# Optimization experiments

Measured on AMD Instinct MI355X. Metric: run time of the kernel, lower is better.

The kernel has to match this reference:

```python
import jax, jax.numpy as jnp
import numpy as np

NP_, NB_, E_, BE_ = 10000, 30000, 300000, 8192
PIN, BIN, EA = 128, 128, 16
HID, GH = 64, 4
D, TH, L, NC, SEQ = 128, 4, 2, 10, 6


def _ln(x, g, b, eps=1e-5):
    m = x.mean(-1, keepdims=True)
    v = ((x - m) ** 2).mean(-1, keepdims=True)
    return (x - m) * jax.lax.rsqrt(v + eps) * g + b


def _seg_softmax(e, seg, n):
    m = jax.ops.segment_max(e, seg, num_segments=n)
    m = jnp.where(jnp.isfinite(m), m, 0.0)
    ex = jnp.exp(e - m[seg])
    s = jax.ops.segment_sum(ex, seg, num_segments=n)
    return ex / (s[seg] + 1e-16)


def _gatv2(xs, xd, es, ed, ea, Wl, bl, Wr, br, We, att, bias, n_dst):
    # PyG GATv2Conv, concat=False, add_self_loops=False, eval mode (no dropout)
    xl = (xs @ Wl + bl).reshape(-1, GH, HID)   # [Ns,H,C] source transform (message content)
    xr = (xd @ Wr + br).reshape(-1, GH, HID)   # [Nd,H,C] dest transform
    eh = (ea @ We).reshape(-1, GH, HID)        # [E,H,C] edge transform (no bias in PyG)
    msg = xl[es] + xr[ed] + eh                 # [E,H,C]
    score = jnp.einsum('ehc,hc->eh', jax.nn.leaky_relu(msg, 0.2), att)
    alpha = _seg_softmax(score, ed, n_dst)     # softmax over in-edges per dest node
    out = jax.ops.segment_sum(alpha[..., None] * xl[es], ed, num_segments=n_dst)
    return out.mean(axis=1) + bias             # concat=False -> mean over heads


def _mha(x, Wqkv, bqkv, Wo, bo):
    S, d = x.shape
    dh = d // TH
    q, k, v = jnp.split(x @ Wqkv + bqkv, 3, axis=-1)
    q = q.reshape(S, TH, dh).transpose(1, 0, 2)
    k = k.reshape(S, TH, dh).transpose(1, 0, 2)
    v = v.reshape(S, TH, dh).transpose(1, 0, 2)
    a = jax.nn.softmax(jnp.einsum('hqd,hkd->hqk', q, k) / jnp.sqrt(jnp.float32(dh)), axis=-1)
    o = jnp.einsum('hqk,hkd->hqd', a, v).transpose(1, 0, 2).reshape(S, d)
    return o @ Wo + bo


def _forward(pitcher_feat, batter_feat, edge_attr, history_states,
             Wp, bp, Wb, bb,
             rel_Wl, rel_bl, rel_Wr, rel_br, rel_We, rel_att, rel_bias,
             rev_Wl, rev_bl, rev_Wr, rev_br, rev_We, rev_att, rev_bias,
             Wgs, bgs, Wet, bet, pos,
             Wqkv, bqkv, Wo, bo, ln1g, ln1b, W1, b1, W2, b2, ln2g, ln2b,
             Wc1, bc1, Wc2, bc2,
             edge_src, edge_dst, edge_ids):
    gelu = lambda t: jax.nn.gelu(t, approximate=False)
    px = gelu(pitcher_feat @ Wp + bp)
    bx = gelu(batter_feat @ Wb + bb)
    # ('pitcher','faces','batter'): messages pitcher->batter, aggregated at batter nodes
    h_b = gelu(_gatv2(px, bx, edge_src, edge_dst, edge_attr,
                      rel_Wl, rel_bl, rel_Wr, rel_br, rel_We, rel_att, rel_bias, bx.shape[0]))
    # reversed relation: batter->pitcher, aggregated at pitcher nodes
    h_p = gelu(_gatv2(bx, px, edge_dst, edge_src, edge_attr,
                      rev_Wl, rev_bl, rev_Wr, rev_br, rev_We, rev_att, rev_bias, px.shape[0]))
    state = jnp.concatenate([h_p.mean(0), h_b.mean(0), edge_attr.mean(0)], -1) @ Wgs + bgs
    tok = jnp.concatenate([h_p[edge_src[edge_ids]], h_b[edge_dst[edge_ids]],
                           edge_attr[edge_ids]], -1) @ Wet + bet
    x = jnp.concatenate([history_states, state[None]], 0) + pos[:SEQ]
    for i in range(L):  # post-LN TransformerEncoderLayer, gelu activation, eval (no dropout)
        x = _ln(x + _mha(x, Wqkv[i], bqkv[i], Wo[i], bo[i]), ln1g[i], ln1b[i])
        f = gelu(x @ W1[i] + b1[i]) @ W2[i] + b2[i]
        x = _ln(x + f, ln2g[i], ln2b[i])
    ctx = x[-1]
    cat = jnp.concatenate([tok, jnp.broadcast_to(ctx, (tok.shape[0], D))], -1)
    return gelu(cat @ Wc1 + bc1) @ Wc2 + bc2


def setup_inputs() -> dict:
    key = jax.random.key(0)
    ks = iter(jax.random.split(key, 64))
    nrm = lambda shape, s: jax.random.normal(next(ks), shape, dtype=jnp.float32) * s
    d = {
        'pitcher_feat': nrm((NP_, PIN), 1.0),
        'batter_feat': nrm((NB_, BIN), 1.0),
        'edge_attr': nrm((E_, EA), 1.0),
        'history_states': nrm((SEQ - 1, D), 1.0),
        'Wp': nrm((PIN, HID), 0.05), 'bp': jnp.zeros((HID,), jnp.float32),
        'Wb': nrm((BIN, HID), 0.05), 'bb': jnp.zeros((HID,), jnp.float32),
    }
    for p in ('rel', 'rev'):
        d[p + '_Wl'] = nrm((HID, GH * HID), 0.05)
        d[p + '_bl'] = jnp.zeros((GH * HID,), jnp.float32)
        d[p + '_Wr'] = nrm((HID, GH * HID), 0.05)
        d[p + '_br'] = jnp.zeros((GH * HID,), jnp.float32)
        d[p + '_We'] = nrm((EA, GH * HID), 0.05)
        d[p + '_att'] = nrm((GH, HID), 0.05)
        d[p + '_bias'] = jnp.zeros((HID,), jnp.float32)
    cin = 2 * HID + EA
    d['Wgs'] = nrm((cin, D), 0.05); d['bgs'] = jnp.zeros((D,), jnp.float32)
    d['Wet'] = nrm((cin, D), 0.05); d['bet'] = jnp.zeros((D,), jnp.float32)
    d['pos'] = nrm((SEQ, D), 0.02)
    d['Wqkv'] = nrm((L, D, 3 * D), 0.05); d['bqkv'] = jnp.zeros((L, 3 * D), jnp.float32)
    d['Wo'] = nrm((L, D, D), 0.05); d['bo'] = jnp.zeros((L, D), jnp.float32)
    d['ln1g'] = jnp.ones((L, D), jnp.float32); d['ln1b'] = jnp.zeros((L, D), jnp.float32)
    d['W1'] = nrm((L, D, 4 * D), 0.05); d['b1'] = jnp.zeros((L, 4 * D), jnp.float32)
    d['W2'] = nrm((L, 4 * D, D), 0.05); d['b2'] = jnp.zeros((L, D), jnp.float32)
    d['ln2g'] = jnp.ones((L, D), jnp.float32); d['ln2b'] = jnp.zeros((L, D), jnp.float32)
    d['Wc1'] = nrm((2 * D, D), 0.05); d['bc1'] = jnp.zeros((D,), jnp.float32)
    d['Wc2'] = nrm((D, NC), 0.05); d['bc2'] = jnp.zeros((NC,), jnp.float32)
    d['edge_src'] = jax.random.randint(next(ks), (E_,), 0, NP_)
    d['edge_dst'] = jax.random.randint(next(ks), (E_,), 0, NB_)
    d['edge_ids'] = jax.random.randint(next(ks), (BE_,), 0, E_)
    return d


def reference(pitcher_feat, batter_feat, edge_attr, history_states,
              Wp, bp, Wb, bb,
              rel_Wl, rel_bl, rel_Wr, rel_br, rel_We, rel_att, rel_bias,
              rev_Wl, rev_bl, rev_Wr, rev_br, rev_We, rev_att, rev_bias,
              Wgs, bgs, Wet, bet, pos,
              Wqkv, bqkv, Wo, bo, ln1g, ln1b, W1, b1, W2, b2, ln2g, ln2b,
              Wc1, bc1, Wc2, bc2,
              edge_src, edge_dst, edge_ids):
    return _forward(pitcher_feat, batter_feat, edge_attr, history_states,
                    Wp, bp, Wb, bb,
                    rel_Wl, rel_bl, rel_Wr, rel_br, rel_We, rel_att, rel_bias,
                    rev_Wl, rev_bl, rev_Wr, rev_br, rev_We, rev_att, rev_bias,
                    Wgs, bgs, Wet, bet, pos,
                    Wqkv, bqkv, Wo, bo, ln1g, ln1b, W1, b1, W2, b2, ln2g, ln2b,
                    Wc1, bc1, Wc2, bc2,
                    edge_src, edge_dst, edge_ids)
```

## Files before the change

### kernel.cpp

```cpp
#include <hip/hip_runtime.h>
#include <math.h>

#define NP 10000
#define NB 30000
#define NEDGE 300000
#define BEDGE 8192
#define EAD 16
#define HID 64
#define GH 4
#define CW 256
#define DD 128
#define SEQ 6
#define NCLS 10
#define L 2
#define NEACOL 64

#if defined(__has_builtin)
#  if __has_builtin(__builtin_amdgcn_fdot2)
#    define HAVE_DOT2 1
#  else
#    define HAVE_DOT2 0
#  endif
#else
#  define HAVE_DOT2 0
// ... 214 lines not shown
  return __builtin_bit_cast(int, __builtin_amdgcn_cvt_pkrtz(fv.x, fv.y));
}
#define GAT_PAIR(X0, X1, EV0, EV1, V1OK, P0MASK)                             \
  {                                                                          \
    float x0 = b2f(X0.x), x1 = b2f(X0.y), x2 = b2f(X0.z), x3 = b2f(X0.w);    \
    float y0 = b2f(X1.x), y1 = b2f(X1.y), y2 = b2f(X1.z), y3 = b2f(X1.w);    \
    float h00 = x0 + r0, h01 = x1 + r1, h02 = x2 + r2, h03 = x3 + r3;        \
    float h10 = y0 + r0, h11 = y1 + r1, h12 = y2 + r2, h13 = y3 + r3;        \
    _Pragma("unroll")                                                        \
    for (int j = 0; j < 8; ++j){                                             \
      int c0 = __builtin_amdgcn_readlane(EV0, j);                            \
      int c1 = __builtin_amdgcn_readlane(EV1, j);                            \
      h16x2 e0 = __builtin_bit_cast(h16x2, c0);                              \
      h16x2 e1 = __builtin_bit_cast(h16x2, c1);                              \
      int4 wr = *(const int4*)&sWeH[j*CW + 4*l];                             \
      h16x2 w0 = __builtin_bit_cast(h16x2, wr.x);                            \
      h16x2 w1 = __builtin_bit_cast(h16x2, wr.y);                            \
      h16x2 w2 = __builtin_bit_cast(h16x2, wr.z);                            \
      h16x2 w3 = __builtin_bit_cast(h16x2, wr.w);                            \
      h00 = __builtin_amdgcn_fdot2(e0, w0, h00, false);                      \
      h01 = __builtin_amdgcn_fdot2(e0, w1, h01, false);                      \
      h02 = __builtin_amdgcn_fdot2(e0, w2, h02, false);                      \
      h03 = __builtin_amdgcn_fdot2(e0, w3, h03, false);                      \
      h10 = __builtin_amdgcn_fdot2(e1, w0, h10, false);                      \
      h11 = __builtin_amdgcn_fdot2(e1, w1, h11, false);                      \
      h12 = __builtin_amdgcn_fdot2(e1, w2, h12, false);                      \
      h13 = __builtin_amdgcn_fdot2(e1, w3, h13, false);                      \
    }                                                                        \
    h00 = fmaxf(h00, 0.2f*h00) * at.x;                                       \
    h01 = fmaxf(h01, 0.2f*h01) * at.y;                                       \
    h02 = fmaxf(h02, 0.2f*h02) * at.z;                                       \
    h03 = fmaxf(h03, 0.2f*h03) * at.w;                                       \
    h10 = fmaxf(h10, 0.2f*h10) * at.x;                                       \
    h11 = fmaxf(h11, 0.2f*h11) * at.y;                                       \
    h12 = fmaxf(h12, 0.2f*h12) * at.z;                                       \
    h13 = fmaxf(h13, 0.2f*h13) * at.w;                                       \
    float g0 = (h00 + h01) + (h02 + h03);                                    \
    float g1 = (h10 + h11) + (h12 + h13);                                    \
    _Pragma("unroll")                                                        \
    for (int off = 1; off < 16; off <<= 1){                                  \
      g0 += __shfl_xor(g0, off);                                             \
      g1 += __shfl_xor(g1, off);                                             \
    }                                                                        \
    float p0 = (P0MASK) ? __expf(g0) : 0.f;                                  \
    float p1 = (V1OK) ? __expf(g1) : 0.f;                                    \
    s += p0 + p1;                                                            \
    a0 = fmaf(p0, x0, fmaf(p1, y0, a0));                                     \
    a1 = fmaf(p0, x1, fmaf(p1, y1, a1));                                     \
    a2 = fmaf(p0, x2, fmaf(p1, y2, a2));                                     \
    a3 = fmaf(p0, x3, fmaf(p1, y3, a3));                                     \
  }
#else
typedef float evt_t;
__device__ __forceinline__ float evload(const float* __restrict__ ea, int e, int l){
  return ea[(size_t)e*EAD + (l & 15)];
}
#define GAT_PAIR(X0, X1, EV0, EV1, V1OK, P0MASK)                             \
  {                                                                          \
    float x0 = b2f(X0.x), x1 = b2f(X0.y), x2 = b2f(X0.z), x3 = b2f(X0.w);    \
    float y0 = b2f(X1.x), y1 = b2f(X1.y), y2 = b2f(X1.z), y3 = b2f(X1.w);    \
    float h00 = x0 + r0, h01 = x1 + r1, h02 = x2 + r2, h03 = x3 + r3;        \
    float h10 = y0 + r0, h11 = y1 + r1, h12 = y2 + r2, h13 = y3 + r3;        \
    int ia0 = __float_as_int(EV0);                                           \
    int ia1 = __float_as_int(EV1);                                           \
    _Pragma("unroll")                                                        \
    for (int k = 0; k < EAD; ++k){                                           \
      float c0 = __int_as_float(__builtin_amdgcn_readlane(ia0, k));          \
      float c1 = __int_as_float(__builtin_amdgcn_readlane(ia1, k));          \
      float4 wv = *(const float4*)&sWeH[k*CW + 4*l];                         \
      h00 = fmaf(c0, wv.x, h00); h01 = fmaf(c0, wv.y, h01);                  \
      h02 = fmaf(c0, wv.z, h02); h03 = fmaf(c0, wv.w, h03);                  \
      h10 = fmaf(c1, wv.x, h10); h11 = fmaf(c1, wv.y, h11);                  \
      h12 = fmaf(c1, wv.z, h12); h13 = fmaf(c1, wv.w, h13);                  \
    }                                                                        \
    h00 = fmaxf(h00, 0.2f*h00) * at.x;                                       \
    h01 = fmaxf(h01, 0.2f*h01) * at.y;                                       \
    h02 = fmaxf(h02, 0.2f*h02) * at.z;                                       \
    h03 = fmaxf(h03, 0.2f*h03) * at.w;                                       \
    h10 = fmaxf(h10, 0.2f*h10) * at.x;                                       \
    h11 = fmaxf(h11, 0.2f*h11) * at.y;                                       \
    h12 = fmaxf(h12, 0.2f*h12) * at.z;                                       \
    h13 = fmaxf(h13, 0.2f*h13) * at.w;                                       \
    float g0 = (h00 + h01) + (h02 + h03);                                    \
    float g1 = (h10 + h11) + (h12 + h13);                                    \
    _Pragma("unroll")                                                        \
    for (int off = 1; off < 16; off <<= 1){                                  \
      g0 += __shfl_xor(g0, off);                                             \
      g1 += __shfl_xor(g1, off);                                             \
    }                                                                        \
    float p0 = (P0MASK) ? __expf(g0) : 0.f;                                  \
    float p1 = (V1OK) ? __expf(g1) : 0.f;                                    \
    s += p0 + p1;                                                            \
    a0 = fmaf(p0, x0, fmaf(p1, y0, a0));                                     \
    a1 = fmaf(p0, x1, fmaf(p1, y1, a1));                                     \
    a2 = fmaf(p0, x2, fmaf(p1, y2, a2));                                     \
    a3 = fmaf(p0, x3, fmaf(p1, y3, a3));                                     \
  }
#endif

__global__ __launch_bounds__(256)
void gat2_kernel(const unsigned short* __restrict__ xlA_, const unsigned short* __restrict__ xrA_,
                 const float* __restrict__ WeA, const float* __restrict__ attA,
                 const float* __restrict__ biasA, const int2* __restrict__ csrA_,
                 const int* __restrict__ rsA_, float* __restrict__ houtA,
                 const unsigned short* __restrict__ xlB_, const unsigned short* __restrict__ xrB_,
                 const float* __restrict__ WeB, const float* __restrict__ attB,
                 const float* __restrict__ biasB, const int2* __restrict__ csrB_,
                 const int* __restrict__ rsB_, float* __restrict__ houtB,
                 const float* __restrict__ ea, float* __restrict__ mvec, int gsplit)
{
#if HAVE_DOT2
  __shared__ int sWeH[8*CW];
#else
  __shared__ float sWeH[16*CW];
#endif
  __shared__ float csum[4][16][4];
  int t = threadIdx.x, l = t & 63;
  int b = blockIdx.x;
  if (b < NEACOL){
    colsum_seg(b, NEACOL, (const float4*)ea, (long)NEDGE*EAD/4, 4,
               mvec + 128, 1.f/NEDGE, &csum[0][0][0]);
    return;
  }
  b -= NEACOL;
  int ngat = (int)gridDim.x - NEACOL;
  bool isA = b < gsplit;
  const unsigned short* xl = isA ? xlA_ : xlB_;
  const unsigned short* xr = isA ? xrA_ : xrB_;
  const float* We   = isA ? WeA   : WeB;
  const float* att  = isA ? attA  : attB;
  const float* bias = isA ? biasA : biasB;
  const int2* csr   = isA ? csrA_ : csrB_;
  const int* row_start = isA ? rsA_ : rsB_;
  float* hout = isA ? houtA : houtB;
  int ndst = isA ? NB : NP;
  int bid  = isA ? b : b - gsplit;
  int nblk = isA ? gsplit : ngat - gsplit;

#if HAVE_DOT2
  for (int i = t; i < 8*CW; i += 256){
    int j = i >> 8, c = i & 255;
    sWeH[i] = __builtin_bit_cast(int,
        __builtin_amdgcn_cvt_pkrtz(We[(2*j)*CW + c], We[(2*j+1)*CW + c]));
  }
#else
  for (int i = t*4; i < 16*CW; i += 1024)
    *(float4*)&sWeH[i] = *(const float4*)&We[i];
#endif
  __syncthreads();
  float4 at = *(const float4*)&att[4*l];
  float4 bi = *(const float4*)&bias[(l & 15)*4];
  float cs0 = 0.f, cs1 = 0.f, cs2 = 0.f, cs3 = 0.f;
  int wid = bid*4 + (t >> 6);
  int nw = nblk*4;
  for (int d = wid; d < ndst; d += nw){
    ushort4 ru = *(const ushort4*)(xr + (size_t)d*CW + 4*l);
    float r0 = b2f(ru.x), r1 = b2f(ru.y), r2 = b2f(ru.z), r3 = b2f(ru.w);
    int rs = row_start[d], re = row_start[d+1];
    float s = 0.f;
    float a0 = 0.f, a1 = 0.f, a2 = 0.f, a3 = 0.f;
    if (rs < re){
      int last = re - 1;
      #define CLMP(x) ((x) > last ? last : (x))
      int2 qA0 = csr[rs],         qA1 = csr[CLMP(rs+1)];
      int2 qB0 = csr[CLMP(rs+2)], qB1 = csr[CLMP(rs+3)];
      int2 nA0 = csr[CLMP(rs+4)], nA1 = csr[CLMP(rs+5)];
      int2 nB0 = csr[CLMP(rs+6)], nB1 = csr[CLMP(rs+7)];
      ushort4 xA0 = *(const ushort4*)(xl + (size_t)qA0.y*CW + 4*l);
      ushort4 xA1 = *(const ushort4*)(xl + (size_t)qA1.y*CW + 4*l);
      evt_t  evA0 = evload(ea, qA0.x, l);
      evt_t  evA1 = evload(ea, qA1.x, l);
      ushort4 xB0 = *(const ushort4*)(xl + (size_t)qB0.y*CW + 4*l);
      ushort4 xB1 = *(const ushort4*)(xl + (size_t)qB1.y*CW + 4*l);
      evt_t  evB0 = evload(ea, qB0.x, l);
      evt_t  evB1 = evload(ea, qB1.x, l);
      for (int i = rs; i < re; i += 4){
        int2 mA0 = csr[CLMP(i+8)],  mA1 = csr[CLMP(i+9)];
        int2 mB0 = csr[CLMP(i+10)], mB1 = csr[CLMP(i+11)];
        GAT_PAIR(xA0, xA1, evA0, evA1, (i+1 < re), true);
        xA0 = *(const ushort4*)(xl + (size_t)nA0.y*CW + 4*l);
        xA1 = *(const ushort4*)(xl + (size_t)nA1.y*CW + 4*l);
        evA0 = evload(ea, nA0.x, l);
        evA1 = evload(ea, nA1.x, l);
        nA0 = mA0; nA1 = mA1;
        GAT_PAIR(xB0, xB1, evB0, evB1, (i+3 < re), (i+2 < re));
        xB0 = *(const ushort4*)(xl + (size_t)nB0.y*CW + 4*l);
        xB1 = *(const ushort4*)(xl + (size_t)nB1.y*CW + 4*l);
        evB0 = evload(ea, nB0.x, l);
        evB1 = evload(ea, nB1.x, l);
        nB0 = mB0; nB1 = mB1;
      }
      #undef CLMP
    }
    float inv = 1.f / (s + 1e-16f);
    float v0 = a0*inv, v1 = a1*inv, v2 = a2*inv, v3 = a3*inv;
    v0 += __shfl_xor(v0, 16); v1 += __shfl_xor(v1, 16);
    v2 += __shfl_xor(v2, 16); v3 += __shfl_xor(v3, 16);
    v0 += __shfl_xor(v0, 32); v1 += __shfl_xor(v1, 32);
    v2 += __shfl_xor(v2, 32); v3 += __shfl_xor(v3, 32);
    if (l < 16){
      float4 o;
      o.x = geluf(v0*0.25f + bi.x);
      o.y = geluf(v1*0.25f + bi.y);
      o.z = geluf(v2*0.25f + bi.z);
      o.w = geluf(v3*0.25f + bi.w);
      *(float4*)(hout + (size_t)d*HID + 4*l) = o;
      cs0 += o.x; cs1 += o.y; cs2 += o.z; cs3 += o.w;
    }
  }
  int w = t >> 6;
  if (l < 16){
    csum[w][l][0] = cs0; csum[w][l][1] = cs1;
    csum[w][l][2] = cs2; csum[w][l][3] = cs3;
  }
  __syncthreads();
  if (t < 64){
    int lq = t >> 2, j = t & 3;
    float sum = csum[0][lq][j] + csum[1][lq][j] + csum[2][lq][j] + csum[3][lq][j];
    float scale = isA ? (1.f/NB) : (1.f/NP);
    float* dst = isA ? (mvec + 64) : mvec;
    atomicAdd(&dst[t], sum * scale);
  }
}

__device__ void gemmcat_body(int bid, const float* __restrict__ hp, const float* __restrict__ hb,
                             const float* __restrict__ ea, const int* __restrict__ esrc,
                             const int* __restrict__ edst, const int* __restrict__ eids,
                             const float* __restrict__ W, const float* __restrict__ bias,
                             float* __restrict__ out)
{
  __shared__ float sAT[16][68];
  __shared__ float sB[16][68];
  __shared__ int sS[64], sD[64], sE[64];
  int t = threadIdx.x;
  int m0 = (bid >> 1)*64, n0 = (bid & 1)*64;
  if (t < 64){
    int e = eids[m0 + t];
    sS[t] = esrc[e]; sD[t] = edst[e]; sE[t] = e;
  }
  __syncthreads();
  int tr = t >> 4, tc = t & 15;
  float acc[4][4] = {};
  for (int k0 = 0; k0 < 144; k0 += 16){
    {
      int r = t >> 2, c = (t & 3) * 4;
      const float* src; int col = k0 + c;
      if (k0 < 64)       { src = hp + (size_t)sS[r]*HID; }
      else if (k0 < 128) { src = hb + (size_t)sD[r]*HID; col -= 64; }
      else               { src = ea + (size_t)sE[r]*EAD; col -= 128; }
      float4 va = *(const float4*)(src + col);
      sAT[c+0][r] = va.x; sAT[c+1][r] = va.y; sAT[c+2][r] = va.z; sAT[c+3][r] = va.w;
    }
    {
      int r = t >> 4, c = (t & 15) * 4;
      float4 vb = *(const float4*)(W + (size_t)(k0+r)*DD + n0 + c);
      *(float4*)&sB[r][c] = vb;
    }
    __syncthreads();
    #pragma unroll
    for (int k = 0; k < 16; ++k){
      float4 av = *(const float4*)&sAT[k][tr*4];
      float4 bv = *(const float4*)&sB[k][tc*4];
      acc[0][0] = fmaf(av.x, bv.x, acc[0][0]);
      acc[0][1] = fmaf(av.x, bv.y, acc[0][1]);
      acc[0][2] = fmaf(av.x, bv.z, acc[0][2]);
      acc[0][3] = fmaf(av.x, bv.w, acc[0][3]);
      acc[1][0] = fmaf(av.y, bv.x, acc[1][0]);
      acc[1][1] = fmaf(av.y, bv.y, acc[1][1]);
      acc[1][2] = fmaf(av.y, bv.z, acc[1][2]);
      acc[1][3] = fmaf(av.y, bv.w, acc[1][3]);
      acc[2][0] = fmaf(av.z, bv.x, acc[2][0]);
      acc[2][1] = fmaf(av.z, bv.y, acc[2][1]);
      acc[2][2] = fmaf(av.z, bv.z, acc[2][2]);
      acc[2][3] = fmaf(av.z, bv.w, acc[2][3]);
      acc[3][0] = fmaf(av.w, bv.x, acc[3][0]);
      acc[3][1] = fmaf(av.w, bv.y, acc[3][1]);
      acc[3][2] = fmaf(av.w, bv.z, acc[3][2]);
      acc[3][3] = fmaf(av.w, bv.w, acc[3][3]);
    }
    __syncthreads();
  }
  #pragma unroll
  for (int i = 0; i < 4; ++i){
    int gr = m0 + tr*4 + i;
    float4 v;
    v.x = acc[i][0] + bias[n0 + tc*4 + 0];
    v.y = acc[i][1] + bias[n0 + tc*4 + 1];
    v.z = acc[i][2] + bias[n0 + tc*4 + 2];
    v.w = acc[i][3] + bias[n0 + tc*4 + 3];
    *(float4*)(out + (size_t)gr*DD + n0 + tc*4) = v;
  }
}

__global__ __launch_bounds__(256)
void gemmcat_kernel(const float* __restrict__ hp, const float* __restrict__ hb,
                    const float* __restrict__ ea, const int* __restrict__ esrc,
                    const int* __restrict__ edst, const int* __restrict__ eids,
                    const float* __restrict__ Wet, const float* __restrict__ bet,
                    float* __restrict__ tokb)
{
  gemmcat_body(blockIdx.x, hp, hb, ea, esrc, edst, eids, Wet, bet, tokb);
}

template<int K, int N, int NC>
__device__ __forceinline__ void qstageF(const float* __restrict__ x,
                                        const float* __restrict__ W,
                                        float (&a)[6][4], int q, int ch)
{
  constexpr int NQ = N/4;
  constexpr int KC = K/NC;
  constexpr int J  = KC/4;
  const float4* wp = (const float4*)W + (size_t)(ch*KC)*NQ + q;
  const float* xb = x + ch*KC;
  float4 wv[KC];
  int kx[J];
  #pragma unroll
  for (int j = 0; j < J; ++j){
    int k4 = (j + ch) & (J-1);
    kx[j] = k4;
    wv[j*4+0] = wp[(size_t)(k4*4+0)*NQ];
    wv[j*4+1] = wp[(size_t)(k4*4+1)*NQ];
    wv[j*4+2] = wp[(size_t)(k4*4+2)*NQ];
    wv[j*4+3] = wp[(size_t)(k4*4+3)*NQ];
  }
  #pragma unroll
  for (int s = 0; s < 6; ++s){ a[s][0]=0.f; a[s][1]=0.f; a[s][2]=0.f; a[s][3]=0.f; }
  #pragma unroll
  for (int j = 0; j < J; ++j){
    #pragma unroll
    for (int s = 0; s < 6; ++s){
      float4 xv = *(const float4*)&xb[s*K + kx[j]*4];
      a[s][0]=fmaf(xv.x,wv[j*4+0].x,a[s][0]); a[s][0]=fmaf(xv.y,wv[j*4+1].x,a[s][0]);
      a[s][0]=fmaf(xv.z,wv[j*4+2].x,a[s][0]); a[s][0]=fmaf(xv.w,wv[j*4+3].x,a[s][0]);
      a[s][1]=fmaf(xv.x,wv[j*4+0].y,a[s][1]); a[s][1]=fmaf(xv.y,wv[j*4+1].y,a[s][1]);
      a[s][1]=fmaf(xv.z,wv[j*4+2].y,a[s][1]); a[s][1]=fmaf(xv.w,wv[j*4+3].y,a[s][1]);
      a[s][2]=fmaf(xv.x,wv[j*4+0].z,a[s][2]); a[s][2]=fmaf(xv.y,wv[j*4+1].z,a[s][2]);
      a[s][2]=fmaf(xv.z,wv[j*4+2].z,a[s][2]); a[s][2]=fmaf(xv.w,wv[j*4+3].z,a[s][2]);
      a[s][3]=fmaf(xv.x,wv[j*4+0].w,a[s][3]); a[s][3]=fmaf(xv.y,wv[j*4+1].w,a[s][3]);
      a[s][3]=fmaf(xv.z,wv[j*4+2].w,a[s][3]); a[s][3]=fmaf(xv.w,wv[j*4+3].w,a[s][3]);
    }
  }
  #pragma unroll
  for (int off = 1; off < NC; off <<= 1){
    #pragma unroll
    for (int s = 0; s < 6; ++s){
      a[s][0]+=__shfl_xor(a[s][0],off); a[s][1]+=__shfl_xor(a[s][1],off);
      a[s][2]+=__shfl_xor(a[s][2],off); a[s][3]+=__shfl_xor(a[s][3],off);
    }
  }
}

__global__ __launch_bounds__(512)
void xform_kernel(const float* __restrict__ hist, const float* __restrict__ mvec,
                  const float* __restrict__ Wgs, const float* __restrict__ bgs,
                  const float* __restrict__ pos,
                  const float* __restrict__ Wqkv, const float* __restrict__ bqkv,
                  const float* __restrict__ Wo, const float* __restrict__ bo,
                  const float* __restrict__ ln1g, const float* __restrict__ ln1b,
                  const float* __restrict__ W1, const float* __restrict__ b1,
                  const float* __restrict__ W2, const float* __restrict__ b2,
                  const float* __restrict__ ln2g, const float* __restrict__ ln2b,
                  const float* __restrict__ Wc1, const float* __restrict__ bc1,
                  float* __restrict__ bias2)
{
  __shared__ float sx[SEQ*DD];
  __shared__ float sq[SEQ*3*DD];
  __shared__ float sh[SEQ*512];
  __shared__ float st[SEQ*DD];
  __shared__ float sc[4][6][6];
  __shared__ float smv[144];
  int t = threadIdx.x;

  for (int i = t; i < (SEQ-1)*DD; i += 512) sx[i] = hist[i] + pos[i];
  if (t < 144) smv[t] = mvec[t];
  __syncthreads();
  if (t < 256){
    int q = t >> 3, ch = t & 7;
    float4 wv[18];
    #pragma unroll
    for (int kk = 0; kk < 18; ++kk)
      wv[kk] = *(const float4*)&Wgs[(ch*18+kk)*DD + q*4];
    float a0=0.f,a1=0.f,a2=0.f,a3=0.f;
    #pragma unroll
    for (int kk = 0; kk < 18; ++kk){
      float xv = smv[ch*18+kk];
      a0=fmaf(xv,wv[kk].x,a0); a1=fmaf(xv,wv[kk].y,a1);
      a2=fmaf(xv,wv[kk].z,a2); a3=fmaf(xv,wv[kk].w,a3);
    }
    #pragma unroll
    for (int off = 1; off < 8; off <<= 1){
      a0+=__shfl_xor(a0,off); a1+=__shfl_xor(a1,off);
      a2+=__shfl_xor(a2,off); a3+=__shfl_xor(a3,off);
    }
    if (ch == 0){
      int n = q*4, base = (SEQ-1)*DD + n;
      sx[base+0]=a0+bgs[n+0]+pos[base+0];
      sx[base+1]=a1+bgs[n+1]+pos[base+1];
      sx[base+2]=a2+bgs[n+2]+pos[base+2];
      sx[base+3]=a3+bgs[n+3]+pos[base+3];
    }
  }
  __syncthreads();

  for (int lyr = 0; lyr < L; ++lyr){
    if (t < 384){
      int q = t >> 2, ch = t & 3;
      const float* wq = Wqkv + (size_t)lyr*DD*3*DD;
      const float* bq = bqkv + lyr*3*DD;
      float a[6][4];
      qstageF<128,384,4>(sx, wq, a, q, ch);
      if (ch == 0){
        int n = q*4;
        #pragma unroll
        for (int s = 0; s < 6; ++s){
          sq[s*384+n+0]=a[s][0]+bq[n+0];
          sq[s*384+n+1]=a[s][1]+bq[n+1];
          sq[s*384+n+2]=a[s][2]+bq[n+2];
          sq[s*384+n+3]=a[s][3]+bq[n+3];
        }
      }
    }
    __syncthreads();
    if (t < 144){
      int h = t/36, r = t%36, qi = r/6, ki = r%6;
      float acc = 0.f;
      #pragma unroll
      for (int d2 = 0; d2 < 32; ++d2)
        acc = fmaf(sq[qi*384 + h*32 + d2], sq[ki*384 + 128 + h*32 + d2], acc);
      sc[h][qi][ki] = acc * 0.17677669529663687f;
    }
    __syncthreads();
    if (t < 24){
      int h = t/6, qi = t%6;
      float* row = sc[h][qi];
      float mx = row[0];
      #pragma unroll
      for (int k = 1; k < 6; ++k) mx = fmaxf(mx, row[k]);
      float sm = 0.f;
      #pragma unroll
      for (int k = 0; k < 6; ++k){ row[k] = __expf(row[k]-mx); sm += row[k]; }
      float inv = 1.f/sm;
      #pragma unroll
      for (int k = 0; k < 6; ++k) row[k] *= inv;
    }
    __syncthreads();
    for (int i = t; i < SEQ*DD; i += 512){
      int s = i >> 7, n = i & 127, h = n >> 5, d2 = n & 31;
      float acc = 0.f;
      #pragma unroll
      for (int ki = 0; ki < 6; ++ki)
        acc = fmaf(sc[h][s][ki], sq[ki*384 + 256 + h*32 + d2], acc);
      st[i] = acc;
    }
    __syncthreads();
    {
      int q = t >> 4, ch = t & 15;
      float a[6][4];
      qstageF<128,128,16>(st, Wo + (size_t)lyr*DD*DD, a, q, ch);
      if (ch == 0){
        int n = q*4;
        const float* bop = bo + lyr*DD;
        #pragma unroll
        for (int s = 0; s < 6; ++s){
          sh[s*128+n+0]=a[s][0]+bop[n+0]+sx[s*128+n+0];
          sh[s*128+n+1]=a[s][1]+bop[n+1]+sx[s*128+n+1];
          sh[s*128+n+2]=a[s][2]+bop[n+2]+sx[s*128+n+2];
          sh[s*128+n+3]=a[s][3]+bop[n+3]+sx[s*128+n+3];
        }
      }
    }
    __syncthreads();
    {
      int w = t >> 6, lw = t & 63;
      if (w < SEQ){
        const float* g = ln1g + lyr*DD; const float* be = ln1b + lyr*DD;
        float v0 = sh[w*DD + lw], v1 = sh[w*DD + 64 + lw];
        float sm = v0 + v1;
        #pragma unroll
        for (int off = 1; off < 64; off <<= 1) sm += __shfl_xor(sm, off);
        float mean = sm * 0.0078125f;
        float d0 = v0-mean, d1 = v1-mean;
        float qv = d0*d0 + d1*d1;
        #pragma unroll
        for (int off = 1; off < 64; off <<= 1) qv += __shfl_xor(qv, off);
        float inv = rsqrtf(qv*0.0078125f + 1e-5f);
        sx[w*DD + lw]      = d0*inv*g[lw] + be[lw];
        sx[w*DD + 64 + lw] = d1*inv*g[64+lw] + be[64+lw];
      }
    }
    __syncthreads();
    {
      int q = t >> 2, ch = t & 3;
      const float* w1 = W1 + (size_t)lyr*DD*512;
      const float* b1p = b1 + lyr*512;
      float a[6][4];
      qstageF<128,512,4>(sx, w1, a, q, ch);
      if (ch == 0){
        int n = q*4;
        #pragma unroll
        for (int s = 0; s < 6; ++s){
          sh[s*512+n+0]=geluf(a[s][0]+b1p[n+0]);
          sh[s*512+n+1]=geluf(a[s][1]+b1p[n+1]);
          sh[s*512+n+2]=geluf(a[s][2]+b1p[n+2]);
          sh[s*512+n+3]=geluf(a[s][3]+b1p[n+3]);
        }
      }
    }
    __syncthreads();
    {
      int q = t >> 4, ch = t & 15;
      const float* w2 = W2 + (size_t)lyr*512*DD;
      const float* b2p = b2 + lyr*DD;
      float a[6][4];
      qstageF<512,128,16>(sh, w2, a, q, ch);
      if (ch == 0){
        int n = q*4;
        #pragma unroll
        for (int s = 0; s < 6; ++s){
          st[s*128+n+0]=a[s][0]+b2p[n+0]+sx[s*128+n+0];
          st[s*128+n+1]=a[s][1]+b2p[n+1]+sx[s*128+n+1];
          st[s*128+n+2]=a[s][2]+b2p[n+2]+sx[s*128+n+2];
          st[s*128+n+3]=a[s][3]+b2p[n+3]+sx[s*128+n+3];
        }
      }
    }
    __syncthreads();
    {
      int w = t >> 6, lw = t & 63;
      if (w < SEQ){
        const float* g = ln2g + lyr*DD; const float* be = ln2b + lyr*DD;
        float v0 = st[w*DD + lw], v1 = st[w*DD + 64 + lw];
        float sm = v0 + v1;
        #pragma unroll
        for (int off = 1; off < 64; off <<= 1) sm += __shfl_xor(sm, off);
        float mean = sm * 0.0078125f;
        float d0 = v0-mean, d1 = v1-mean;
        float qv = d0*d0 + d1*d1;
        #pragma unroll
        for (int off = 1; off < 64; off <<= 1) qv += __shfl_xor(qv, off);
        float inv = rsqrtf(qv*0.0078125f + 1e-5f);
        sx[w*DD + lw]      = d0*inv*g[lw] + be[lw];
        sx[w*DD + 64 + lw] = d1*inv*g[64+lw] + be[64+lw];
      }
    }
    __syncthreads();
  }
  if (t < 256){
    int q = t >> 3, ch = t & 7;
    const float4* wp = (const float4*)(Wc1 + (size_t)DD*DD) + (size_t)(ch*16)*32 + q;
    const float* xb = &sx[(SEQ-1)*DD + ch*16];
    float4 wv[16];
    int kx[4];
    #pragma unroll
    for (int j = 0; j < 4; ++j){
      int k4 = (j + ch) & 3;
      kx[j] = k4;
      wv[j*4+0] = wp[(size_t)(k4*4+0)*32];
      wv[j*4+1] = wp[(size_t)(k4*4+1)*32];
      wv[j*4+2] = wp[(size_t)(k4*4+2)*32];
      wv[j*4+3] = wp[(size_t)(k4*4+3)*32];
    }
    float a0=0.f,a1=0.f,a2=0.f,a3=0.f;
    #pragma unroll
    for (int j = 0; j < 4; ++j){
      float4 xv = *(const float4*)&xb[kx[j]*4];
      a0=fmaf(xv.x,wv[j*4+0].x,a0); a0=fmaf(xv.y,wv[j*4+1].x,a0);
      a0=fmaf(xv.z,wv[j*4+2].x,a0); a0=fmaf(xv.w,wv[j*4+3].x,a0);
      a1=fmaf(xv.x,wv[j*4+0].y,a1); a1=fmaf(xv.y,wv[j*4+1].y,a1);
      a1=fmaf(xv.z,wv[j*4+2].y,a1); a1=fmaf(xv.w,wv[j*4+3].y,a1);
      a2=fmaf(xv.x,wv[j*4+0].z,a2); a2=fmaf(xv.y,wv[j*4+1].z,a2);
      a2=fmaf(xv.z,wv[j*4+2].z,a2); a2=fmaf(xv.w,wv[j*4+3].z,a2);
      a3=fmaf(xv.x,wv[j*4+0].w,a3); a3=fmaf(xv.y,wv[j*4+1].w,a3);
      a3=fmaf(xv.z,wv[j*4+2].w,a3); a3=fmaf(xv.w,wv[j*4+3].w,a3);
    }
    #pragma unroll
    for (int off = 1; off < 8; off <<= 1){
      a0+=__shfl_xor(a0,off); a1+=__shfl_xor(a1,off);
      a2+=__shfl_xor(a2,off); a3+=__shfl_xor(a3,off);
    }
    if (ch == 0){
      int n = q*4;
      bias2[n+0]=a0+bc1[n+0];
      bias2[n+1]=a1+bc1[n+1];
      bias2[n+2]=a2+bc1[n+2];
      bias2[n+3]=a3+bc1[n+3];
    }
  }
}

__global__ __launch_bounds__(256)
void cls_kernel(const float* __restrict__ A, const float* __restrict__ W,
                const float* __restrict__ bias2, const float* __restrict__ Wc2,
                const float* __restrict__ bc2, float* __restrict__ out)
{
  __shared__ float sAT[16][68];
  __shared__ float sB[16][132];
  __shared__ float sH[64][129];
  int t = threadIdx.x;
  int m0 = blockIdx.x * 64;
  int tr = t >> 4, tc = t & 15;
  float acc[4][8] = {};
  for (int k0 = 0; k0 < DD; k0 += 16){
    {
      int r = t >> 2, c = (t & 3) * 4;
      float4 va = *(const float4*)(A + (size_t)(m0+r)*DD + k0 + c);
      sAT[c+0][r] = va.x; sAT[c+1][r] = va.y; sAT[c+2][r] = va.z; sAT[c+3][r] = va.w;
    }
    {
      int r = t >> 4, c = (t & 15) * 8;
      float4 b0 = *(const float4*)(W + (size_t)(k0+r)*DD + c);
      float4 b1 = *(const float4*)(W + (size_t)(k0+r)*DD + c + 4);
      *(float4*)&sB[r][c] = b0;
      *(float4*)&sB[r][c+4] = b1;
    }
    __syncthreads();
    #pragma unroll
    for (int k = 0; k < 16; ++k){
      float4 av = *(const float4*)&sAT[k][tr*4];
      float4 b0 = *(const float4*)&sB[k][tc*8];
      float4 b1 = *(const float4*)&sB[k][tc*8+4];
      #pragma unroll
      for (int i = 0; i < 4; ++i){
        float avi = (i==0)?av.x:(i==1)?av.y:(i==2)?av.z:av.w;
        acc[i][0] = fmaf(avi, b0.x, acc[i][0]);
        acc[i][1] = fmaf(avi, b0.y, acc[i][1]);
        acc[i][2] = fmaf(avi, b0.z, acc[i][2]);
        acc[i][3] = fmaf(avi, b0.w, acc[i][3]);
        acc[i][4] = fmaf(avi, b1.x, acc[i][4]);
        acc[i][5] = fmaf(avi, b1.y, acc[i][5]);
        acc[i][6] = fmaf(avi, b1.z, acc[i][6]);
        acc[i][7] = fmaf(avi, b1.w, acc[i][7]);
      }
    }
    __syncthreads();
  }
  #pragma unroll
  for (int i = 0; i < 4; ++i){
    #pragma unroll
    for (int j = 0; j < 8; ++j){
      sH[tr*4+i][tc*8+j] = geluf(acc[i][j] + bias2[tc*8+j]);
    }
  }
  __syncthreads();
  if (t < 64){
    float a10[NCLS];
    #pragma unroll
    for (int c = 0; c < NCLS; ++c) a10[c] = bc2[c];
    for (int k = 0; k < DD; ++k){
      float hv = sH[t][k];
      #pragma unroll
      for (int c = 0; c < NCLS; ++c)
        a10[c] = fmaf(hv, Wc2[k*NCLS + c], a10[c]);
    }
    #pragma unroll
    for (int c = 0; c < NCLS; ++c)
      out[(size_t)(m0+t)*NCLS + c] = a10[c];
  }
}

extern "C" void kernel_launch(void* const* d_in, const int* in_sizes, int n_in,
                              void* d_out, int out_size, void* d_ws, size_t ws_size,
                              hipStream_t stream){
  (void)in_sizes; (void)n_in; (void)out_size; (void)ws_size;
  const float* pitcher = (const float*)d_in[0];
  const float* batter  = (const float*)d_in[1];
  const float* eattr   = (const float*)d_in[2];
  const float* hist    = (const float*)d_in[3];
  const float* Wp = (const float*)d_in[4];
  const float* bp = (const float*)d_in[5];
  const float* Wb = (const float*)d_in[6];
  const float* bb = (const float*)d_in[7];
  const float* rel_Wl  = (const float*)d_in[8];
  const float* rel_bl  = (const float*)d_in[9];
  const float* rel_Wr  = (const float*)d_in[10];
  const float* rel_br  = (const float*)d_in[11];
  const float* rel_We  = (const float*)d_in[12];
  const float* rel_att = (const float*)d_in[13];
  const float* rel_bias= (const float*)d_in[14];
  const float* rev_Wl  = (const float*)d_in[15];
  const float* rev_bl  = (const float*)d_in[16];
  const float* rev_Wr  = (const float*)d_in[17];
  const float* rev_br  = (const float*)d_in[18];
  const float* rev_We  = (const float*)d_in[19];
  const float* rev_att = (const float*)d_in[20];
  const float* rev_bias= (const float*)d_in[21];
  const float* Wgs = (const float*)d_in[22];
  const float* bgs = (const float*)d_in[23];
  const float* Wet = (const float*)d_in[24];
  const float* bet = (const float*)d_in[25];
  const float* pos = (const float*)d_in[26];
  const float* Wqkv= (const float*)d_in[27];
  const float* bqkv= (const float*)d_in[28];
  const float* Wo  = (const float*)d_in[29];
  const float* bo  = (const float*)d_in[30];
  const float* ln1g= (const float*)d_in[31];
  const float* ln1b= (const float*)d_in[32];
  const float* W1  = (const float*)d_in[33];
  const float* b1  = (const float*)d_in[34];
  const float* W2  = (const float*)d_in[35];
  const float* b2  = (const float*)d_in[36];
  const float* ln2g= (const float*)d_in[37];
  const float* ln2b= (const float*)d_in[38];
  const float* Wc1 = (const float*)d_in[39];
  const float* bc1 = (const float*)d_in[40];
  const float* Wc2 = (const float*)d_in[41];
  const float* bc2 = (const float*)d_in[42];
  const int* esrc = (const int*)d_in[43];
  const int* edst = (const int*)d_in[44];
  const int* eids = (const int*)d_in[45];

  char* w = (char*)d_ws;
  size_t off = 0;
  auto alloc = [&](size_t bytes)->void*{
    void* p = (void*)(w + off);
    off += (bytes + 255) & ~(size_t)255;
    return p;
  };
  unsigned short* px_bf  = (unsigned short*)alloc((size_t)NP*HID*2);
  unsigned short* bx_bf  = (unsigned short*)alloc((size_t)NB*HID*2);
  float*          hp     = (float*)alloc((size_t)NP*HID*4);
  float*          hb     = (float*)alloc((size_t)NB*HID*4);
  unsigned short* xlA    = (unsigned short*)alloc((size_t)NP*CW*2);
  unsigned short* xrA    = (unsigned short*)alloc((size_t)NB*CW*2);
  unsigned short* xlB    = (unsigned short*)alloc((size_t)NB*CW*2);
  unsigned short* xrB    = (unsigned short*)alloc((size_t)NP*CW*2);
  int*            degAB  = (int*)alloc((size_t)(NB+NP)*4);
  int*            degA   = degAB;
  int*            degB   = degAB + NB;
  int*            rowstA = (int*)alloc((size_t)(NB+1)*4);
  int*            rowstB = (int*)alloc((size_t)(NP+1)*4);
  int*            cursA  = (int*)alloc((size_t)NB*4);
  int*            cursB  = (int*)alloc((size_t)NP*4);
  int2*           csrA   = (int2*)alloc((size_t)NEDGE*8);
  int2*           csrB   = (int2*)alloc((size_t)NEDGE*8);
  float*          mvec   = (float*)alloc(144*4);
  float*          bias2  = (float*)alloc(DD*4);
  float*          tokb   = (float*)xlA;

  const int nbCount = (NEDGE + 255)/256;
  const int nbP = (NP + 63)/64;
  const int nbB = (NB + 63)/64;

  hipMemsetAsync(degAB, 0, (size_t)(NB+NP)*4, stream);
  k1_count_enc<<<nbCount + nbP + nbB, 256, 0, stream>>>(
      edst, esrc, degA, degB,
      pitcher, Wp, bp, px_bf, batter, Wb, bb, bx_bf, nbCount, nbP);

  scan2_kernel<<<2, 1024, 0, stream>>>(degA, rowstA, cursA, NB,
                                       degB, rowstB, cursB, NP, mvec);

  k2_scatter_proj<<<nbCount + 2*nbP + 2*nbB, 256, 0, stream>>>(
      edst, esrc, cursA, cursB, csrA, csrB, px_bf, bx_bf,
      rel_Wl, rel_bl, rel_Wr, rel_br, rev_Wl, rev_bl, rev_Wr, rev_br,
      xlA, xrA, xlB, xrB, nbCount, nbP, nbB);

  gat2_kernel<<<NEACOL + 4096, 256, 0, stream>>>(
      xlA, xrA, rel_We, rel_att, rel_bias, csrA, rowstA, hb,
      xlB, xrB, rev_We, rev_att, rev_bias, csrB, rowstB, hp,
      eattr, mvec, 2048);

  gemmcat_kernel<<<256, 256, 0, stream>>>(
      hp, hb, eattr, esrc, edst, eids, Wet, bet, tokb);

  xform_kernel<<<1, 512, 0, stream>>>(
      hist, mvec, Wgs, bgs, pos, Wqkv, bqkv, Wo, bo, ln1g, ln1b,
      W1, b1, W2, b2, ln2g, ln2b, Wc1, bc1, bias2);

  cls_kernel<<<BEDGE/64, 256, 0, stream>>>(tokb, Wc1, bias2, Wc2, bc2, (float*)d_out);
}
```

Measured before the change: 389.0 us.

## Stage transformer weights through padded shared memory with 1024-thread xform block

The single-block transformer kernel now runs 1024 threads and loads each weight matrix in chunks with coalesced float4 reads into a padded shared-memory tile. Each thread then accumulates from shared memory instead of holding many float4 weights in registers loaded with strided global accesses. This is meant to cut register pressure and improve global load coalescing and parallelism in the serial single-block stage. The cost is many extra __syncthreads per GEMM and around 67KB of shared memory.

Result: slower. 397.5 us (+2.2%).

```diff
diff --git a/kernel.cpp b/kernel.cpp
--- a/kernel.cpp
+++ b/kernel.cpp
@@ -540,55 +540,43 @@
   gemmcat_body(blockIdx.x, hp, hb, ea, esrc, edst, eids, Wet, bet, tokb);
 }
 
-template<int K, int N, int NC>
-__device__ __forceinline__ void qstageF(const float* __restrict__ x,
-                                        const float* __restrict__ W,
-                                        float (&a)[6][4], int q, int ch)
-{
-  constexpr int NQ = N/4;
-  constexpr int KC = K/NC;
-  constexpr int J  = KC/4;
-  const float4* wp = (const float4*)W + (size_t)(ch*KC)*NQ + q;
-  const float* xb = x + ch*KC;
-  float4 wv[KC];
-  int kx[J];
+template<int NQ, int ROUNDS>
+__device__ __forceinline__ void stageW(const float* __restrict__ g, float4* __restrict__ s,
+                                       int t){
+  float4 tmp[ROUNDS];
   #pragma unroll
-  for (int j = 0; j < J; ++j){
-    int k4 = (j + ch) & (J-1);
-    kx[j] = k4;
-    wv[j*4+0] = wp[(size_t)(k4*4+0)*NQ];
-    wv[j*4+1] = wp[(size_t)(k4*4+1)*NQ];
-    wv[j*4+2] = wp[(size_t)(k4*4+2)*NQ];
-    wv[j*4+3] = wp[(size_t)(k4*4+3)*NQ];
-  }
+  for (int r = 0; r < ROUNDS; ++r)
+    tmp[r] = ((const float4*)g)[t + r*1024];
   #pragma unroll
-  for (int s = 0; s < 6; ++s){ a[s][0]=0.f; a[s][1]=0.f; a[s][2]=0.f; a[s][3]=0.f; }
+  for (int r = 0; r < ROUNDS; ++r){
+    int idx = t + r*1024;
+    int row = idx / NQ, c4 = idx - row*NQ;
+    s[row*(NQ+1) + c4] = tmp[r];
+  }
+}
+
+template<int K, int N>
+__device__ __forceinline__ void qaccL(const float* __restrict__ x, int xk0,
+                                      const float4* __restrict__ sW4, int wrow0,
+                                      float (&a)[6][4], int q){
+  constexpr int NQ1 = N/4 + 1;
+  const float4* wp = sW4 + (size_t)wrow0*NQ1 + q;
+  float4 w0 = wp[0], w1 = wp[NQ1], w2 = wp[2*NQ1], w3 = wp[3*NQ1];
   #pragma unroll
-  for (int j = 0; j < J; ++j){
-    #pragma unroll
-    for (int s = 0; s < 6; ++s){
-      float4 xv = *(const float4*)&xb[s*K + kx[j]*4];
-      a[s][0]=fmaf(xv.x,wv[j*4+0].x,a[s][0]); a[s][0]=fmaf(xv.y,wv[j*4+1].x,a[s][0]);
-      a[s][0]=fmaf(xv.z,wv[j*4+2].x,a[s][0]); a[s][0]=fmaf(xv.w,wv[j*4+3].x,a[s][0]);
-      a[s][1]=fmaf(xv.x,wv[j*4+0].y,a[s][1]); a[s][1]=fmaf(xv.y,wv[j*4+1].y,a[s][1]);
-      a[s][1]=fmaf(xv.z,wv[j*4+2].y,a[s][1]); a[s][1]=fmaf(xv.w,wv[j*4+3].y,a[s][1]);
-      a[s][2]=fmaf(xv.x,wv[j*4+0].z,a[s][2]); a[s][2]=fmaf(xv.y,wv[j*4+1].z,a[s][2]);
-      a[s][2]=fmaf(xv.z,wv[j*4+2].z,a[s][2]); a[s][2]=fmaf(xv.w,wv[j*4+3].z,a[s][2]);
-      a[s][3]=fmaf(xv.x,wv[j*4+0].w,a[s][3]); a[s][3]=fmaf(xv.y,wv[j*4+1].w,a[s][3]);
-      a[s][3]=fmaf(xv.z,wv[j*4+2].w,a[s][3]); a[s][3]=fmaf(xv.w,wv[j*4+3].w,a[s][3]);
-    }
-  }
-  #pragma unroll
-  for (int off = 1; off < NC; off <<= 1){
-    #pragma unroll
-    for (int s = 0; s < 6; ++s){
-      a[s][0]+=__shfl_xor(a[s][0],off); a[s][1]+=__shfl_xor(a[s][1],off);
-      a[s][2]+=__shfl_xor(a[s][2],off); a[s][3]+=__shfl_xor(a[s][3],off);
-    }
-  }
-}
-
-__global__ __launch_bounds__(512)
+  for (int s = 0; s < 6; ++s){
+    float4 xv = *(const float4*)&x[s*K + xk0];
+    a[s][0]=fmaf(xv.x,w0.x,a[s][0]); a[s][0]=fmaf(xv.y,w1.x,a[s][0]);
+    a[s][0]=fmaf(xv.z,w2.x,a[s][0]); a[s][0]=fmaf(xv.w,w3.x,a[s][0]);
+    a[s][1]=fmaf(xv.x,w0.y,a[s][1]); a[s][1]=fmaf(xv.y,w1.y,a[s][1]);
+    a[s][1]=fmaf(xv.z,w2.y,a[s][1]); a[s][1]=fmaf(xv.w,w3.y,a[s][1]);
+    a[s][2]=fmaf(xv.x,w0.z,a[s][2]); a[s][2]=fmaf(xv.y,w1.z,a[s][2]);
+    a[s][2]=fmaf(xv.z,w2.z,a[s][2]); a[s][2]=fmaf(xv.w,w3.z,a[s][2]);
+    a[s][3]=fmaf(xv.x,w0.w,a[s][3]); a[s][3]=fmaf(xv.y,w1.w,a[s][3]);
+    a[s][3]=fmaf(xv.z,w2.w,a[s][3]); a[s][3]=fmaf(xv.w,w3.w,a[s][3]);
+  }
+}
+
+__global__ __launch_bounds__(1024)
 void xform_kernel(const float* __restrict__ hist, const float* __restrict__ mvec,
                   const float* __restrict__ Wgs, const float* __restrict__ bgs,
                   const float* __restrict__ pos,
@@ -601,6 +589,7 @@
                   const float* __restrict__ Wc1, const float* __restrict__ bc1,
                   float* __restrict__ bias2)
 {
+  __shared__ float4 sW4[4224];
   __shared__ float sx[SEQ*DD];
   __shared__ float sq[SEQ*3*DD];
   __shared__ float sh[SEQ*512];
@@ -609,21 +598,17 @@
   __shared__ float smv[144];
   int t = threadIdx.x;
 
-  for (int i = t; i < (SEQ-1)*DD; i += 512) sx[i] = hist[i] + pos[i];
-  if (t < 144) smv[t] = mvec[t];
+  if (t < (SEQ-1)*DD) sx[t] = hist[t] + pos[t];
+  if (t >= 1024-144) smv[t-(1024-144)] = mvec[t-(1024-144)];
   __syncthreads();
   if (t < 256){
     int q = t >> 3, ch = t & 7;
-    float4 wv[18];
-    #pragma unroll
-    for (int kk = 0; kk < 18; ++kk)
-      wv[kk] = *(const float4*)&Wgs[(ch*18+kk)*DD + q*4];
     float a0=0.f,a1=0.f,a2=0.f,a3=0.f;
-    #pragma unroll
     for (int kk = 0; kk < 18; ++kk){
+      float4 wv = *(const float4*)&Wgs[(ch*18+kk)*DD + q*4];
       float xv = smv[ch*18+kk];
-      a0=fmaf(xv,wv[kk].x,a0); a1=fmaf(xv,wv[kk].y,a1);
-      a2=fmaf(xv,wv[kk].z,a2); a3=fmaf(xv,wv[kk].w,a3);
+      a0=fmaf(xv,wv.x,a0); a1=fmaf(xv,wv.y,a1);
+      a2=fmaf(xv,wv.z,a2); a3=fmaf(xv,wv.w,a3);
     }
     #pragma unroll
     for (int off = 1; off < 8; off <<= 1){
@@ -641,20 +626,36 @@
   __syncthreads();
 
   for (int lyr = 0; lyr < L; ++lyr){
-    if (t < 384){
-      int q = t >> 2, ch = t & 3;
+    {
       const float* wq = Wqkv + (size_t)lyr*DD*3*DD;
-      const float* bq = bqkv + lyr*3*DD;
-      float a[6][4];
-      qstageF<128,384,4>(sx, wq, a, q, ch);
-      if (ch == 0){
-        int n = q*4;
+      int q = t >> 3, ch = t & 7;
+      float a[6][4] = {};
+      #pragma unroll
+      for (int c = 0; c < 4; ++c){
+        __syncthreads();
+        stageW<96,3>(wq + c*32*384, sW4, t);
+        __syncthreads();
+        if (t < 768) qaccL<128,384>(sx, c*32 + ch*4, sW4, ch*4, a, q);
+      }
+      if (t < 768){
         #pragma unroll
-        for (int s = 0; s < 6; ++s){
-          sq[s*384+n+0]=a[s][0]+bq[n+0];
-          sq[s*384+n+1]=a[s][1]+bq[n+1];
-          sq[s*384+n+2]=a[s][2]+bq[n+2];
-          sq[s*384+n+3]=a[s][3]+bq[n+3];
+        for (int off = 1; off < 8; off <<= 1){
+          #pragma unroll
+          for (int s = 0; s < 6; ++s){
+            a[s][0]+=__shfl_xor(a[s][0],off); a[s][1]+=__shfl_xor(a[s][1],off);
+            a[s][2]+=__shfl_xor(a[s][2],off); a[s][3]+=__shfl_xor(a[s][3],off);
+          }
+        }
+        if (ch == 0){
+          const float* bq = bqkv + lyr*3*DD;
+          int n = q*4;
+          #pragma unroll
+          for (int s = 0; s < 6; ++s){
+            sq[s*384+n+0]=a[s][0]+bq[n+0];
+            sq[s*384+n+1]=a[s][1]+bq[n+1];
+            sq[s*384+n+2]=a[s][2]+bq[n+2];
+            sq[s*384+n+3]=a[s][3]+bq[n+3];
+          }
         }
       }
     }
@@ -682,28 +683,44 @@
       for (int k = 0; k < 6; ++k) row[k] *= inv;
     }
     __syncthreads();
-    for (int i = t; i < SEQ*DD; i += 512){
-      int s = i >> 7, n = i & 127, h = n >> 5, d2 = n & 31;
+    if (t < SEQ*DD){
+      int s2 = t >> 7, n = t & 127, h = n >> 5, d2 = n & 31;
       float acc = 0.f;
       #pragma unroll
       for (int ki = 0; ki < 6; ++ki)
-        acc = fmaf(sc[h][s][ki], sq[ki*384 + 256 + h*32 + d2], acc);
-      st[i] = acc;
-    }
-    __syncthreads();
+        acc = fmaf(sc[h][s2][ki], sq[ki*384 + 256 + h*32 + d2], acc);
+      st[t] = acc;
+    }
     {
+      const float* wo = Wo + (size_t)lyr*DD*DD;
       int q = t >> 4, ch = t & 15;
-      float a[6][4];
-      qstageF<128,128,16>(st, Wo + (size_t)lyr*DD*DD, a, q, ch);
-      if (ch == 0){
-        int n = q*4;
-        const float* bop = bo + lyr*DD;
+      float a[6][4] = {};
+      #pragma unroll
+      for (int c = 0; c < 2; ++c){
+        __syncthreads();
+        stageW<32,2>(wo + c*64*128, sW4, t);
+        __syncthreads();
+        if (t < 512) qaccL<128,128>(st, c*64 + ch*4, sW4, ch*4, a, q);
+      }
+      if (t < 512){
         #pragma unroll
-        for (int s = 0; s < 6; ++s){
-          sh[s*128+n+0]=a[s][0]+bop[n+0]+sx[s*128+n+0];
-          sh[s*128+n+1]=a[s][1]+bop[n+1]+sx[s*128+n+1];
-          sh[s*128+n+2]=a[s][2]+bop[n+2]+sx[s*128+n+2];
-          sh[s*128+n+3]=a[s][3]+bop[n+3]+sx[s*128+n+3];
+        for (int off = 1; off < 16; off <<= 1){
+          #pragma unroll
+          for (int s = 0; s < 6; ++s){
+            a[s][0]+=__shfl_xor(a[s][0],off); a[s][1]+=__shfl_xor(a[s][1],off);
+            a[s][2]+=__shfl_xor(a[s][2],off); a[s][3]+=__shfl_xor(a[s][3],off);
+          }
+        }
+        if (ch == 0){
+          const float* bop = bo + lyr*DD;
+          int n = q*4;
+          #pragma unroll
+          for (int s = 0; s < 6; ++s){
+            sh[s*128+n+0]=a[s][0]+bop[n+0]+sx[s*128+n+0];
+            sh[s*128+n+1]=a[s][1]+bop[n+1]+sx[s*128+n+1];
+            sh[s*128+n+2]=a[s][2]+bop[n+2]+sx[s*128+n+2];
+            sh[s*128+n+3]=a[s][3]+bop[n+3]+sx[s*128+n+3];
+          }
         }
       }
     }
@@ -726,14 +743,27 @@
         sx[w*DD + 64 + lw] = d1*inv*g[64+lw] + be[64+lw];
       }
     }
-    __syncthreads();
     {
-      int q = t >> 2, ch = t & 3;
       const float* w1 = W1 + (size_t)lyr*DD*512;
-      const float* b1p = b1 + lyr*512;
-      float a[6][4];
-      qstageF<128,512,4>(sx, w1, a, q, ch);
+      int q = t >> 3, ch = t & 7;
+      float a[6][4] = {};
+      #pragma unroll
+      for (int c = 0; c < 4; ++c){
+        __syncthreads();
+        stageW<128,4>(w1 + c*32*512, sW4, t);
+        __syncthreads();
+        qaccL<128,512>(sx, c*32 + ch*4, sW4, ch*4, a, q);
+      }
+      #pragma unroll
+      for (int off = 1; off < 8; off <<= 1){
+        #pragma unroll
+        for (int s = 0; s < 6; ++s){
+          a[s][0]+=__shfl_xor(a[s][0],off); a[s][1]+=__shfl_xor(a[s][1],off);
+          a[s][2]+=__shfl_xor(a[s][2],off); a[s][3]+=__shfl_xor(a[s][3],off);
+        }
+      }
       if (ch == 0){
+        const float* b1p = b1 + lyr*512;
         int n = q*4;
         #pragma unroll
         for (int s = 0; s < 6; ++s){
@@ -746,12 +776,26 @@
     }
     __syncthreads();
     {
-      int q = t >> 4, ch = t & 15;
       const float* w2 = W2 + (size_t)lyr*512*DD;
-      const float* b2p = b2 + lyr*DD;
-      float a[6][4];
-      qstageF<512,128,16>(sh, w2, a, q, ch);
+      int q = t >> 5, ch = t & 31;
+      float a[6][4] = {};
+      #pragma unroll
+      for (int c = 0; c < 4; ++c){
+        __syncthreads();
+        stageW<32,4>(w2 + c*128*128, sW4, t);
+        __syncthreads();
+        qaccL<512,128>(sh, c*128 + ch*4, sW4, ch*4, a, q);
+      }
+      #pragma unroll
+      for (int off = 1; off < 32; off <<= 1){
+        #pragma unroll
+        for (int s = 0; s < 6; ++s){
+          a[s][0]+=__shfl_xor(a[s][0],off); a[s][1]+=__shfl_xor(a[s][1],off);
+          a[s][2]+=__shfl_xor(a[s][2],off); a[s][3]+=__shfl_xor(a[s][3],off);
+        }
+      }
       if (ch == 0){
+        const float* b2p = b2 + lyr*DD;
         int n = q*4;
         #pragma unroll
         for (int s = 0; s < 6; ++s){
@@ -787,29 +831,12 @@
     int q = t >> 3, ch = t & 7;
     const float4* wp = (const float4*)(Wc1 + (size_t)DD*DD) + (size_t)(ch*16)*32 + q;
     const float* xb = &sx[(SEQ-1)*DD + ch*16];
-    float4 wv[16];
-    int kx[4];
-    #pragma unroll
-    for (int j = 0; j < 4; ++j){
-      int k4 = (j + ch) & 3;
-      kx[j] = k4;
-      wv[j*4+0] = wp[(size_t)(k4*4+0)*32];
-      wv[j*4+1] = wp[(size_t)(k4*4+1)*32];
-      wv[j*4+2] = wp[(size_t)(k4*4+2)*32];
-      wv[j*4+3] = wp[(size_t)(k4*4+3)*32];
-    }
     float a0=0.f,a1=0.f,a2=0.f,a3=0.f;
-    #pragma unroll
-    for (int j = 0; j < 4; ++j){
-      float4 xv = *(const float4*)&xb[kx[j]*4];
-      a0=fmaf(xv.x,wv[j*4+0].x,a0); a0=fmaf(xv.y,wv[j*4+1].x,a0);
-      a0=fmaf(xv.z,wv[j*4+2].x,a0); a0=fmaf(xv.w,wv[j*4+3].x,a0);
-      a1=fmaf(xv.x,wv[j*4+0].y,a1); a1=fmaf(xv.y,wv[j*4+1].y,a1);
-      a1=fmaf(xv.z,wv[j*4+2].y,a1); a1=fmaf(xv.w,wv[j*4+3].y,a1);
-      a2=fmaf(xv.x,wv[j*4+0].z,a2); a2=fmaf(xv.y,wv[j*4+1].z,a2);
-      a2=fmaf(xv.z,wv[j*4+2].z,a2); a2=fmaf(xv.w,wv[j*4+3].z,a2);
-      a3=fmaf(xv.x,wv[j*4+0].w,a3); a3=fmaf(xv.y,wv[j*4+1].w,a3);
-      a3=fmaf(xv.z,wv[j*4+2].w,a3); a3=fmaf(xv.w,wv[j*4+3].w,a3);
+    for (int kk = 0; kk < 16; ++kk){
+      float4 wv = wp[(size_t)kk*32];
+      float xv = xb[kk];
+      a0=fmaf(xv,wv.x,a0); a1=fmaf(xv,wv.y,a1);
+      a2=fmaf(xv,wv.z,a2); a3=fmaf(xv,wv.w,a3);
     }
     #pragma unroll
     for (int off = 1; off < 8; off <<= 1){
@@ -1000,7 +1027,7 @@
   gemmcat_kernel<<<256, 256, 0, stream>>>(
       hp, hb, eattr, esrc, edst, eids, Wet, bet, tokb);
 
-  xform_kernel<<<1, 512, 0, stream>>>(
+  xform_kernel<<<1, 1024, 0, stream>>>(
       hist, mvec, Wgs, bgs, pos, Wqkv, bqkv, Wo, bo, ln1g, ln1b,
       W1, b1, W2, b2, ln2g, ln2b, Wc1, bc1, bias2);
 
```
